# Optimization experiments

Hardware: AMD Instinct MI355X
Metric: run time of the kernel (lower is better)

Reference implementation:

```python
import jax, jax.numpy as jnp
import numpy as np

B, D, K = 32768, 256, 4096
BETA = 0.25

def setup_inputs() -> dict:
    key = jax.random.key(0)
    k1, k2 = jax.random.split(key)
    z_e = jax.random.normal(k1, (B, D), dtype=jnp.float32)
    # matches nn.Embedding init: uniform(-1/K, 1/K)
    codebook_weight = jax.random.uniform(k2, (K, D), dtype=jnp.float32,
                                         minval=-1.0 / K, maxval=1.0 / K)
    return {"z_e": z_e, "codebook_weight": codebook_weight}

def reference(z_e, codebook_weight):
    # squared L2 distances [B, K] via expansion: ||z||^2 + ||w||^2 - 2 z.w
    distances = (jnp.sum(z_e ** 2, axis=1, keepdims=True)
                 + jnp.sum(codebook_weight ** 2, axis=1)
                 - 2.0 * z_e @ codebook_weight.T)
    indices = jnp.argmin(distances, axis=1)            # [B] int
    z_q = codebook_weight[indices]                     # [B, D] gather

    codebook_loss = jnp.mean((z_q - jax.lax.stop_gradient(z_e)) ** 2)
    commitment_loss = jnp.mean((z_e - jax.lax.stop_gradient(z_q)) ** 2)
    quant_loss = codebook_loss + BETA * commitment_loss

    # straight-through estimator
    z_q_st = z_e + jax.lax.stop_gradient(z_q - z_e)

    # perplexity: avoid materializing [B, K] one-hot; bincount == one_hot.mean
    counts = jnp.bincount(indices, length=K).astype(jnp.float32)
    avg_probs = counts / z_e.shape[0]
    perplexity = jnp.exp(-jnp.sum(avg_probs * jnp.log(avg_probs + 1e-10)))

    return z_q_st, indices, quant_loss, perplexity
```

## Files before the change

kernel.cpp:

```cpp
#include <hip/hip_runtime.h>
#include <math.h>

constexpr int NROWS = 32768;
constexpr int DIMC  = 256;
constexpr int KC    = 4096;

typedef __attribute__((ext_vector_type(8))) short short8;
typedef __attribute__((ext_vector_type(4))) float f32x4;

#define AS1 __attribute__((address_space(1)))
#define AS3 __attribute__((address_space(3)))

#define WINQ 420u

__device__ __forceinline__ unsigned short f2bf(float x) {
  unsigned u = __float_as_uint(x);
  return (unsigned short)((u + 0x7fffu + ((u >> 16) & 1u)) >> 16);
}

__global__ __launch_bounds__(256)
void vq_prep(const float* __restrict__ Z, const float* __restrict__ W,
             unsigned short* __restrict__ Zh, unsigned short* __restrict__ Wh,
             int* __restrict__ clr) {
  const int t = threadIdx.x;
  if (blockIdx.x == 0) {
#pragma unroll
    for (int i = 0; i < 17; ++i) {
      const int idx = t + i * 256;
      if (idx < 4352) clr[idx] = 0;
    }
  }
  const bool isW = blockIdx.x >= 2048;
  const int bid  = isW ? ((int)blockIdx.x - 2048) : (int)blockIdx.x;
  const float* X = isW ? W : Z;
  unsigned short* out = isW ? Wh : Zh;
  const int blk = bid >> 3;
  const int kb  = bid & 7;

  f32x4 v[2][2];
#pragma unroll
  for (int gi = 0; gi < 2; ++gi) {
    const int g = t + gi * 256;
    const int r = g >> 2, slot = g & 3;
    const int s8 = slot ^ ((r >> 1) & 3);
    const float* src = X + (size_t)(blk * 128 + r) * DIMC + kb * 32 + s8 * 8;
    v[gi][0] = *(const f32x4*)(src);
    v[gi][1] = *(const f32x4*)(src + 4);
  }
#pragma unroll
  for (int gi = 0; gi < 2; ++gi) {
    const int g = t + gi * 256;
    short8 vh;
#pragma unroll
    for (int j = 0; j < 8; ++j) vh[j] = (short)f2bf(v[gi][j >> 2][j & 3]);
    *(short8*)(out + ((size_t)blk * 8 + kb) * 4096 + g * 8) = vh;
  }
}

#define DPP_MIN4(v)                                                            \
  {                                                                            \
    unsigned _t;                                                               \
    _t = (unsigned)__builtin_amdgcn_update_dpp((int)(v), (int)(v), 0x121, 0xF, 0xF, false); \
    (v) = min((v), _t);                                                        \
    _t = (unsigned)__builtin_amdgcn_update_dpp((int)(v), (int)(v), 0x122, 0xF, 0xF, false); \
    (v) = min((v), _t);                                                        \
    _t = (unsigned)__builtin_amdgcn_update_dpp((int)(v), (int)(v), 0x124, 0xF, 0xF, false); \
    (v) = min((v), _t);                                                        \
    _t = (unsigned)__builtin_amdgcn_update_dpp((int)(v), (int)(v), 0x128, 0xF, 0xF, false); \
    (v) = min((v), _t);                                                        \
  }

__global__ __launch_bounds__(256, 4)
void vq_mfma(const unsigned short* __restrict__ Zh, const unsigned short* __restrict__ Wh,
             uint2* __restrict__ partial) {
  __shared__ char lds[16384];
  const int t = threadIdx.x, lane = t & 63, w = t >> 6;
  const int bid = (int)blockIdx.x;
  const int sbid = ((bid & 7) << 10) + (bid >> 3);
  const int rb = sbid >> 5, cb = sbid & 31;
  const int q = lane >> 4, ml = lane & 15;
  const int wr = w >> 1, wc = w & 1;

  const unsigned short* bsrc = Wh + (size_t)cb * 32768 + (w >> 1) * 4096
                             + (w & 1) * 2048 + lane * 8;
  char* bdst = lds + (w >> 1) * 8192 + (w & 1) * 4096;

  int aoff[4], boff[4];
#pragma unroll
  for (int i = 0; i < 4; ++i) {
    const int r = wr * 64 + i * 16 + ml;
    aoff[i] = (r * 4 + (q ^ ((r >> 1) & 3))) * 16;
    const int c = wc * 64 + i * 16 + ml;
    boff[i] = (c * 4 + (q ^ ((c >> 1) & 3))) * 16;
  }
  const char* Abase = (const char*)Zh + (size_t)rb * 65536;

  f32x4 acc[4][4];
#pragma unroll
  for (int i = 0; i < 4; ++i)
#pragma unroll
    for (int j = 0; j < 4; ++j) acc[i][j] = (f32x4){0.f, 0.f, 0.f, 0.f};

  for (int kb2 = 0; kb2 < 4; ++kb2) {
    __syncthreads();
#pragma unroll
    for (int i = 0; i < 4; ++i)
      __builtin_amdgcn_global_load_lds((const AS1 void*)(bsrc + kb2 * 8192 + i * 512),
                                       (AS3 void*)(bdst + i * 1024), 16, 0, 0);
    short8 Af[2][4];
#pragma unroll
    for (int sec = 0; sec < 2; ++sec) {
      const int kb = kb2 * 2 + sec;
#pragma unroll
      for (int i = 0; i < 4; ++i)
        Af[sec][i] = *(const short8*)(Abase + (size_t)kb * 8192 + aoff[i]);
    }
    __syncthreads();
#pragma unroll
    for (int sec = 0; sec < 2; ++sec) {
      short8 Bf[4];
#pragma unroll
      for (int i = 0; i < 4; ++i)
        Bf[i] = *(const short8*)(lds + sec * 8192 + boff[i]);
#pragma unroll
      for (int i = 0; i < 4; ++i)
#pragma unroll
        for (int j = 0; j < 4; ++j)
          acc[i][j] = __builtin_amdgcn_mfma_f32_16x16x32_bf16(Af[sec][i], Bf[j], acc[i][j], 0, 0, 0);
    }
  }

  __syncthreads();
  uint2* pk = (uint2*)lds;
  const float SCN = -4194304.0f;

#pragma unroll
  for (int i = 0; i < 4; ++i) {
#pragma unroll
    for (int r = 0; r < 4; ++r) {
      unsigned k[4];
#pragma unroll
      for (int j = 0; j < 4; ++j) {
        const unsigned qv = (unsigned)fmaf(acc[i][j][r], SCN, 524288.0f);
        k[j] = (qv << 7) + (unsigned)(wc * 64 + j * 16 + ml);
      }
      const unsigned m01 = min(k[0], k[1]), x01 = max(k[0], k[1]);
      const unsigned m23 = min(k[2], k[3]), x23 = max(k[2], k[3]);
      const unsigned k1l = min(m01, m23);
      const unsigned k2l = min(max(m01, m23), min(x01, x23));
      unsigned m1 = k1l;
      DPP_MIN4(m1)
      unsigned c2 = (k1l == m1) ? k2l : k1l;
      DPP_MIN4(c2)
      if (ml == 0) pk[w * 64 + (i * 16 + q * 4 + r)] = make_uint2(m1, c2);
    }
  }
  __syncthreads();
  if (t < 128) {
    const int wrh = t >> 6, lr = t & 63;
    const uint2 A2 = pk[(wrh * 2 + 0) * 64 + lr];
    const uint2 B2 = pk[(wrh * 2 + 1) * 64 + lr];
    const unsigned k1 = min(A2.x, B2.x);
    const unsigned k2 = min(min(A2.y, B2.y), max(A2.x, B2.x));
    const unsigned g1 = ((k1 >> 7) << 12) | ((unsigned)cb << 7) | (k1 & 127u);
    const unsigned g2 = ((k2 >> 7) << 12) | ((unsigned)cb << 7) | (k2 & 127u);
    const int row = rb * 128 + wrh * 64 + lr;
    partial[(size_t)row * 32 + cb] = make_uint2(g1, g2);
  }
}

__device__ __forceinline__ float exact_d(const float* __restrict__ Z,
                                         const float* __restrict__ W,
                                         int row, int c, float a) {
  const float* z = Z + (size_t)row * DIMC;
  const float* w = W + (size_t)c * DIMC;
  float dot = 0.f;
  for (int d0 = 0; d0 < DIMC; d0 += 4) {
    const float4 zv = *(const float4*)(z + d0);
    const float4 wv = *(const float4*)(w + d0);
    dot = fmaf(zv.x, wv.x, dot);
    dot = fmaf(zv.y, wv.y, dot);
    dot = fmaf(zv.z, wv.z, dot);
    dot = fmaf(zv.w, wv.w, dot);
  }
  return a - 2.0f * dot;
}

__global__ __launch_bounds__(256)
void vq_tailA(const float* __restrict__ Z, const float* __restrict__ W,
              const uint2* __restrict__ partial, int* __restrict__ kbuf) {
  const int lane = threadIdx.x & 63, wv = threadIdx.x >> 6;
  const int row = blockIdx.x * 4 + wv;
  const float INF = 3.4e38f;

  unsigned k1 = 0xFFFFFFFFu, k2 = 0xFFFFFFFFu;
  if (lane < 32) {
    const uint2 p = partial[(size_t)row * 32 + lane];
    k1 = p.x; k2 = p.y;
  }
  unsigned g1 = k1, g2 = k2;
#pragma unroll
  for (int mask = 1; mask < 32; mask <<= 1) {
    const unsigned og1 = (unsigned)__shfl_xor((int)g1, mask);
    const unsigned og2 = (unsigned)__shfl_xor((int)g2, mask);
    const unsigned mx = max(g1, og1);
    g1 = min(g1, og1);
    g2 = min(min(g2, og2), mx);
  }
  g1 = (unsigned)__shfl((int)g1, 0);
  g2 = (unsigned)__shfl((int)g2, 0);

  int k;
  const unsigned q1 = g1 >> 12;
  if ((g2 >> 12) - q1 > WINQ) {
    k = (int)(g1 & 4095u);
  } else {
    const float4 z4 = *(const float4*)(Z + (size_t)row * DIMC + lane * 4);
    double ns = (double)z4.x * z4.x + (double)z4.y * z4.y +
                (double)z4.z * z4.z + (double)z4.w * z4.w;
#pragma unroll
    for (int mask = 1; mask < 64; mask <<= 1) ns += __shfl_xor(ns, mask);
    const float a = (float)ns;

    const bool scan   = (lane < 32) && ((k2 >> 12) <= q1 + WINQ);
    const bool single = (lane < 32) && !scan && ((k1 >> 12) <= q1 + WINQ);
    float bd = INF; int bi = 0x7fffffff;
    if (single) {
      const int c = (int)(k1 & 4095u);
      const float d = exact_d(Z, W, row, c, a);
      if (d < bd || (d == bd && c < bi)) { bd = d; bi = c; }
    }
    unsigned long long msk = __ballot(scan);
    while (msk) {
      const int cbk = __ffsll(msk) - 1; msk &= msk - 1;
#pragma unroll
      for (int h = 0; h < 2; ++h) {
        const int c = cbk * 128 + h * 64 + lane;
        const float d = exact_d(Z, W, row, c, a);
        if (d < bd || (d == bd && c < bi)) { bd = d; bi = c; }
      }
    }
#pragma unroll
    for (int mask = 1; mask < 64; mask <<= 1) {
      const float od = __shfl_xor(bd, mask);
      const int   oi = __shfl_xor(bi, mask);
      if (od < bd || (od == bd && oi < bi)) { bd = od; bi = oi; }
    }
    k = bi;
  }
  if (lane == 0) kbuf[row] = k;
}

__global__ __launch_bounds__(256)
void vq_tailB(const float* __restrict__ Z, const float* __restrict__ W,
              const int* __restrict__ kbuf, float* __restrict__ zq_out,
              float* __restrict__ idx_out, double* __restrict__ lossp,
              int* __restrict__ hist) {
  __shared__ double sh[4];
  const int lane = threadIdx.x & 63, wv = threadIdx.x >> 6;
  const int row = blockIdx.x * 4 + wv;

  const int k = kbuf[row];
  const float4 z4 = *(const float4*)(Z + (size_t)row * DIMC + lane * 4);
  const float4 w4 = *(const float4*)(W + (size_t)k   * DIMC + lane * 4);
  *(float4*)(zq_out + (size_t)row * DIMC + lane * 4) = w4;

  const double dx = (double)w4.x - (double)z4.x;
  const double dy = (double)w4.y - (double)z4.y;
  const double dz = (double)w4.z - (double)z4.z;
  const double dw = (double)w4.w - (double)z4.w;
  double l = dx * dx + dy * dy + dz * dz + dw * dw;
#pragma unroll
  for (int off = 32; off > 0; off >>= 1) l += __shfl_down(l, off);

  if (lane == 0) { sh[wv] = l; idx_out[row] = (float)k; atomicAdd(&hist[k], 1); }
  __syncthreads();
  if (threadIdx.x == 0) lossp[blockIdx.x] = sh[0] + sh[1] + sh[2] + sh[3];
}

__global__ __launch_bounds__(1024)
void vq_final(const double* __restrict__ lossp, const int* __restrict__ hist,
              float* __restrict__ scal) {
  __shared__ double sL[16], sH[16];
  const int t = threadIdx.x, lane = t & 63, wv = t >> 6;
  double L = 0.0, H = 0.0;
  for (int i = t; i < NROWS / 4; i += 1024) L += lossp[i];
  for (int k = t; k < KC; k += 1024) {
    const double p = (double)hist[k] / (double)NROWS;
    H -= p * log(p + 1e-10);
  }
#pragma unroll
  for (int off = 32; off > 0; off >>= 1) {
    L += __shfl_down(L, off);
    H += __shfl_down(H, off);
  }
  if (lane == 0) { sL[wv] = L; sH[wv] = H; }
  __syncthreads();
  if (t == 0) {
    double LT = 0.0, HT = 0.0;
#pragma unroll
    for (int i = 0; i < 16; ++i) { LT += sL[i]; HT += sH[i]; }
    scal[0] = (float)(LT * 1.25 / ((double)NROWS * (double)DIMC));
    scal[1] = (float)exp(HT);
  }
}

extern "C" void kernel_launch(void* const* d_in, const int* in_sizes, int n_in,
                              void* d_out, int out_size, void* d_ws, size_t ws_size,
                              hipStream_t stream) {
  const float* Z = (const float*)d_in[0];
  const float* W = (const float*)d_in[1];
  float* out = (float*)d_out;
  float* zq_out  = out;
  float* idx_out = out + (size_t)NROWS * DIMC;
  float* scal    = idx_out + NROWS;

  char* ws = (char*)d_ws;
  int*    hist       = (int*)(ws + 1024);
  int*    kbuf       = (int*)(ws + 262144);
  double* lossp      = (double*)(ws + 524288);
  uint2*  partial    = (uint2*)(ws + 1048576);
  unsigned short* Zh = (unsigned short*)(ws + 20971520);
  unsigned short* Wh = (unsigned short*)(ws + 37748736);

  vq_prep<<<2304, 256, 0, stream>>>(Z, W, Zh, Wh, (int*)ws);
  vq_mfma<<<8192, 256, 0, stream>>>(Zh, Wh, partial);
  vq_tailA<<<NROWS / 4, 256, 0, stream>>>(Z, W, partial, kbuf);
  vq_tailB<<<NROWS / 4, 256, 0, stream>>>(Z, W, kbuf, zq_out, idx_out, lossp, hist);
  vq_final<<<1, 1024, 0, stream>>>(lossp, hist, scal);
}
```

Before: 224.0 us.

## Fuse final reduction into tail kernel via last-block atomic counter; use packed bf16 cvt

Merges the single-block final reduction kernel into the tail kernel. Each block bumps a two-level atomic counter (64 slot counters, then a master counter), and only the last block to finish reads all loss partials and histogram bins to compute the loss and perplexity. This drops one kernel launch and its dependency gap, at the cost of extra atomics and a 256-thread final reduction instead of 1024. It also swaps the manual float-to-bf16 rounding in the prep kernel for the v_cvt_pk_bf16_f32 packed instruction.

```diff
diff --git a/kernel.cpp b/kernel.cpp
--- a/kernel.cpp
+++ b/kernel.cpp
@@ -7,15 +7,16 @@
 
 typedef __attribute__((ext_vector_type(8))) short short8;
 typedef __attribute__((ext_vector_type(4))) float f32x4;
+typedef __attribute__((ext_vector_type(4))) unsigned u32x4;
 
 #define AS1 __attribute__((address_space(1)))
 #define AS3 __attribute__((address_space(3)))
 
 #define WINQ 420u
 
-__device__ __forceinline__ unsigned short f2bf(float x) {
-  unsigned u = __float_as_uint(x);
-  return (unsigned short)((u + 0x7fffu + ((u >> 16) & 1u)) >> 16);
+__device__ __forceinline__ unsigned long long atom_load_u64(const void* p) {
+  return __hip_atomic_load((const unsigned long long*)p, __ATOMIC_RELAXED,
+                           __HIP_MEMORY_SCOPE_AGENT);
 }
 
 __global__ __launch_bounds__(256)
@@ -50,10 +51,16 @@
 #pragma unroll
   for (int gi = 0; gi < 2; ++gi) {
     const int g = t + gi * 256;
-    short8 vh;
-#pragma unroll
-    for (int j = 0; j < 8; ++j) vh[j] = (short)f2bf(v[gi][j >> 2][j & 3]);
-    *(short8*)(out + ((size_t)blk * 8 + kb) * 4096 + g * 8) = vh;
+    u32x4 pk;
+#pragma unroll
+    for (int d = 0; d < 4; ++d) {
+      const float a = v[gi][d >> 1][(d & 1) * 2 + 0];
+      const float c = v[gi][d >> 1][(d & 1) * 2 + 1];
+      unsigned r2;
+      asm("v_cvt_pk_bf16_f32 %0, %1, %2" : "=v"(r2) : "v"(a), "v"(c));
+      pk[d] = r2;
+    }
+    *(u32x4*)(out + ((size_t)blk * 8 + kb) * 4096 + g * 8) = pk;
   }
 }
 
@@ -252,13 +259,17 @@
 }
 
 __global__ __launch_bounds__(256)
-void vq_tailB(const float* __restrict__ Z, const float* __restrict__ W,
-              const int* __restrict__ kbuf, float* __restrict__ zq_out,
-              float* __restrict__ idx_out, double* __restrict__ lossp,
-              int* __restrict__ hist) {
+void vq_tailBF(const float* __restrict__ Z, const float* __restrict__ W,
+               const int* __restrict__ kbuf, float* __restrict__ zq_out,
+               float* __restrict__ idx_out, double* __restrict__ lossp,
+               int* __restrict__ hist, int* __restrict__ slots,
+               int* __restrict__ master, float* __restrict__ scal) {
   __shared__ double sh[4];
+  __shared__ double sLf[4], sHf[4];
+  __shared__ int s_last;
   const int lane = threadIdx.x & 63, wv = threadIdx.x >> 6;
-  const int row = blockIdx.x * 4 + wv;
+  const int b = (int)blockIdx.x;
+  const int row = b * 4 + wv;
 
   const int k = kbuf[row];
   const float4 z4 = *(const float4*)(Z + (size_t)row * DIMC + lane * 4);
@@ -275,18 +286,25 @@
 
   if (lane == 0) { sh[wv] = l; idx_out[row] = (float)k; atomicAdd(&hist[k], 1); }
   __syncthreads();
-  if (threadIdx.x == 0) lossp[blockIdx.x] = sh[0] + sh[1] + sh[2] + sh[3];
-}
-
-__global__ __launch_bounds__(1024)
-void vq_final(const double* __restrict__ lossp, const int* __restrict__ hist,
-              float* __restrict__ scal) {
-  __shared__ double sL[16], sH[16];
-  const int t = threadIdx.x, lane = t & 63, wv = t >> 6;
+  if (threadIdx.x == 0) {
+    lossp[b] = sh[0] + sh[1] + sh[2] + sh[3];
+    __threadfence();
+    int last = 0;
+    if (atomicAdd(&slots[b & 63], 1) == 127) {
+      if (atomicAdd(master, 1) == 63) last = 1;
+    }
+    s_last = last;
+  }
+  __syncthreads();
+  if (!s_last) return;
+
   double L = 0.0, H = 0.0;
-  for (int i = t; i < NROWS / 4; i += 1024) L += lossp[i];
-  for (int k = t; k < KC; k += 1024) {
-    const double p = (double)hist[k] / (double)NROWS;
+  for (int i = threadIdx.x; i < NROWS / 4; i += 256)
+    L += __longlong_as_double((long long)atom_load_u64(&lossp[i]));
+  for (int i = threadIdx.x; i < KC; i += 256) {
+    const int h = __hip_atomic_load(&hist[i], __ATOMIC_RELAXED,
+                                    __HIP_MEMORY_SCOPE_AGENT);
+    const double p = (double)h / (double)NROWS;
     H -= p * log(p + 1e-10);
   }
 #pragma unroll
@@ -294,12 +312,11 @@
     L += __shfl_down(L, off);
     H += __shfl_down(H, off);
   }
-  if (lane == 0) { sL[wv] = L; sH[wv] = H; }
-  __syncthreads();
-  if (t == 0) {
-    double LT = 0.0, HT = 0.0;
-#pragma unroll
-    for (int i = 0; i < 16; ++i) { LT += sL[i]; HT += sH[i]; }
+  if (lane == 0) { sLf[wv] = L; sHf[wv] = H; }
+  __syncthreads();
+  if (threadIdx.x == 0) {
+    const double LT = sLf[0] + sLf[1] + sLf[2] + sLf[3];
+    const double HT = sHf[0] + sHf[1] + sHf[2] + sHf[3];
     scal[0] = (float)(LT * 1.25 / ((double)NROWS * (double)DIMC));
     scal[1] = (float)exp(HT);
   }
@@ -316,6 +333,8 @@
   float* scal    = idx_out + NROWS;
 
   char* ws = (char*)d_ws;
+  int*    slots      = (int*)ws;
+  int*    master     = (int*)(ws + 256);
   int*    hist       = (int*)(ws + 1024);
   int*    kbuf       = (int*)(ws + 262144);
   double* lossp      = (double*)(ws + 524288);
@@ -326,6 +345,6 @@
   vq_prep<<<2304, 256, 0, stream>>>(Z, W, Zh, Wh, (int*)ws);
   vq_mfma<<<8192, 256, 0, stream>>>(Zh, Wh, partial);
   vq_tailA<<<NROWS / 4, 256, 0, stream>>>(Z, W, partial, kbuf);
-  vq_tailB<<<NROWS / 4, 256, 0, stream>>>(Z, W, kbuf, zq_out, idx_out, lossp, hist);
-  vq_final<<<1, 1024, 0, stream>>>(lossp, hist, scal);
-}
+  vq_tailBF<<<NROWS / 4, 256, 0, stream>>>(Z, W, kbuf, zq_out, idx_out,
+                                           lossp, hist, slots, master, scal);
+}
```

After: 463.8 us. 107% more time.
